# Optimization experiments

Measured on AMD Instinct MI355X. Metric: run time of the kernel, lower is better.

The kernel has to match this reference:

```python
import jax, jax.numpy as jnp
import numpy as np

EPS = 1e-14  # clamp floor from torch .clamp(1e-14)


def setup_inputs() -> dict:
    key = jax.random.key(0)
    kq, kk, kv, km = jax.random.split(key, 4)
    B, L, D = 16, 2048, 64
    q = jax.random.normal(kq, (B, L, D), dtype=jnp.float32)
    k = jax.random.normal(kk, (B, L, D), dtype=jnp.float32)
    v = jax.random.normal(kv, (B, L, D), dtype=jnp.float32)
    # boolean mask, True = masked-out position (score forced to 0 in 'dot' mode)
    attn_mask = jax.random.randint(km, (B, L, L), 0, 2).astype(jnp.bool_)
    return {"q": q, "k": k, "v": v, "attn_mask": attn_mask}


def reference(q, k, v, attn_mask):
    # kernel_type='dot': raw QK^T scores (no temperature scaling)
    attn = jnp.einsum('bqd,bkd->bqk', q, k)
    # masked positions set to 0 (not -inf) in the 'dot' path
    attn = jnp.where(attn_mask, jnp.zeros((), attn.dtype), attn)
    # sum-normalization instead of softmax: attn / attn.sum(-1).clamp(1e-14)
    denom = jnp.clip(jnp.sum(attn, axis=2, keepdims=True), EPS)
    attn = attn / denom
    # dropout is identity at inference (eval mode)
    output = jnp.einsum('bqk,bkd->bqd', attn, v)
    return output, attn
```

## Files before the change

### kernel.cpp

```cpp
#include <hip/hip_runtime.h>

#define Bb 16
#define Lq 2048
#define Dd 64
#define QT 32
#define NT 512
#define NWIN 16
#define WINB 32768

typedef _Float16 f16x2 __attribute__((ext_vector_type(2)));
typedef _Float16 f16x8 __attribute__((ext_vector_type(8)));
typedef __attribute__((ext_vector_type(4))) float f32x4;
typedef __attribute__((ext_vector_type(2))) float f32x2;
typedef __attribute__((ext_vector_type(4))) unsigned int u32x4;
typedef __attribute__((ext_vector_type(2))) unsigned int u32x2;
typedef __attribute__((ext_vector_type(4))) int i32x4;
typedef unsigned long long u64;
typedef __attribute__((ext_vector_type(2))) unsigned long long u64x2;

union H8 { f16x8 v8; f16x2 h2[4]; unsigned int u[4]; u32x4 u4; };
union H1 { f16x2 h; unsigned int u; };

__device__ __forceinline__ f16x2 pkrtz(float a, float b) {
  return __builtin_bit_cast(f16x2, __builtin_amdgcn_cvt_pkrtz(a, b));
}
__device__ __forceinline__ f32x4 MF16(f16x8 a, f16x8 b, f32x4 c) {
  return __builtin_amdgcn_mfma_f32_16x16x32_f16(a, b, c, 0, 0, 0);
}
__device__ __forceinline__ f32x4 MFu(u32x4 a, const H8& b, f32x4 c) {
  return MF16(__builtin_bit_cast(f16x8, a), b.v8, c);
}
__device__ __forceinline__ void gl_lds16(const void* g, void* l) {
  __builtin_amdgcn_global_load_lds(
      (const __attribute__((address_space(1))) void*)g,
      (__attribute__((address_space(3))) void*)l, 16, 0, 0);
}

__global__ __launch_bounds__(256)
void sdpa_prep(const float* __restrict__ kg, const float* __restrict__ vg,
               const i32x4* __restrict__ mg4,
               u32x4* __restrict__ Kw4, u32x4* __restrict__ Vq,
               u64* __restrict__ mb)
{
  const int t = threadIdx.x, blk = blockIdx.x;
  if (blk < 1024) {
    const int row = blk * 32 + (t >> 3);
    const int oct = t & 7;
    const int b = row >> 11, r = row & 2047;
    const int win = r >> 7, rw = r & 127;
    const float* kp = kg + (size_t)row * Dd + oct * 8;
    f32x4 a = *(const f32x4*)kp;
    f32x4 c = *(const f32x4*)(kp + 4);
    H1 h0, h1, h2, h3, l0, l1, l2, l3;
    h0.h = pkrtz(a.x, a.y); l0.h = pkrtz(a.x - (float)h0.h.x, a.y - (float)h0.h.y);
    h1.h = pkrtz(a.z, a.w); l1.h = pkrtz(a.z - (float)h1.h.x, a.w - (float)h1.h.y);
    h2.h = pkrtz(c.x, c.y); l2.h = pkrtz(c.x - (float)h2.h.x, c.y - (float)h2.h.y);
    h3.h = pkrtz(c.z, c.w); l3.h = pkrtz(c.z - (float)h3.h.x, c.w - (float)h3.h.y);
    u32x4 hh = {h0.u, h1.u, h2.u, h3.u};
    u32x4 ll = {l0.u, l1.u, l2.u, l3.u};
    const int sl = oct ^ (rw & 7);
    const size_t base = ((size_t)((b * 16 + win) * 128 + rw)) * 16;
    Kw4[base + sl] = hh;
    Kw4[base + 8 + sl] = ll;
  } else if (blk < 2048) {
    const int v_ = (blk - 1024) * 256 + t;
    const int ln = v_ & 15, nt = (v_ >> 4) & 3, u = (v_ >> 6) & 3;
    const int g = (v_ >> 8) & 7, w = (v_ >> 11) & 7, b = v_ >> 14;
    const int R = w * 256 + g * 32 + u * 4;
    const float* vp = vg + ((size_t)b * Lq + R) * Dd + nt * 16 + ln;
    H1 p0, p1, p2, p3;
    p0.h = pkrtz(vp[0 * Dd],  vp[1 * Dd]);
    p1.h = pkrtz(vp[2 * Dd],  vp[3 * Dd]);
    p2.h = pkrtz(vp[16 * Dd], vp[17 * Dd]);
    p3.h = pkrtz(vp[18 * Dd], vp[19 * Dd]);
    u32x4 o = {p0.u, p1.u, p2.u, p3.u};
    Vq[v_] = o;
  } else {
    const int l  = t & 63;
    const int wg = ((blk - 2048) << 2) | (t >> 6);
    i32x4 cur = __builtin_nontemporal_load(&mg4[((size_t)wg * 32) * 64 + l]);
#pragma unroll 1
    for (int it = 0; it < 32; ++it) {
      i32x4 nxt = {0, 0, 0, 0};
      if (it < 31) nxt = __builtin_nontemporal_load(&mg4[((size_t)wg * 32 + it + 1) * 64 + l]);
      u64 b0 = __ballot(cur.x != 0);
      u64 b1 = __ballot(cur.y != 0);
      u64 b2 = __ballot(cur.z != 0);
      u64 b3 = __ballot(cur.w != 0);
      if (l == 0) {
        u64* o = mb + ((size_t)wg * 32 + it) * 4;
        u64x2 w0 = {b0, b1}, w1 = {b2, b3};
        *(u64x2*)o = w0;
        *(u64x2*)(o + 2) = w1;
      }
      cur = nxt;
    }
  }
}

__global__ __launch_bounds__(NT, 4)
void sdpa_main(const float* __restrict__ qg, const char* __restrict__ Kw,
               const u32x4* __restrict__ Vqp, const u64* __restrict__ mbp,
               float* __restrict__ outO, float* __restrict__ outA)
{
  __shared__ char kbuf[2][WINB];
  __shared__ unsigned int Qh[QT][36], Ql[QT][36];
  __shared__ float red[QT][4];
  __shared__ float dinv_s[QT];

  const int tid = threadIdx.x;
  const int l   = tid & 63;
  const int ln  = l & 15;
  const int u   = l >> 4;
  const int w   = tid >> 6;
  const int qt  = w >> 2;
  const int ks  = w & 3;
  const int bid = (int)(blockIdx.x % 8) * 128 + (int)(blockIdx.x / 8);
  const int b   = bid >> 6;
  const int q0  = (bid & 63) * QT;

  {
    int r = tid >> 4, i4 = tid & 15;
    f32x4 qv = *(const f32x4*)(qg + (size_t)(b * Lq + q0 + r) * Dd + 4 * i4);
    H1 ha, hb, la, lb;
    ha.h = pkrtz(qv.x, qv.y); la.h = pkrtz(qv.x - (float)ha.h.x, qv.y - (float)ha.h.y);
    hb.h = pkrtz(qv.z, qv.w); lb.h = pkrtz(qv.z - (float)hb.h.x, qv.w - (float)hb.h.y);
    Qh[r][2 * i4] = ha.u; Qh[r][2 * i4 + 1] = hb.u;
    Ql[r][2 * i4] = la.u; Ql[r][2 * i4 + 1] = lb.u;
  }

  const char* kwb = Kw + (size_t)b * NWIN * WINB;
  auto STAGE = [&](int buf_, int win_) {
#pragma unroll
    for (int i = 0; i < 4; ++i)
      gl_lds16(kwb + (size_t)win_ * WINB + i * 8192 + w * 1024 + l * 16,
               &kbuf[buf_][i * 8192 + w * 1024]);
  };
  STAGE(0, 0);
  __syncthreads();

  H8 Bh0, Bh1, Bl0, Bl1;
  Bh0.u4 = *(const u32x4*)&Qh[16 * qt + ln][4 * u];
  Bh1.u4 = *(const u32x4*)&Qh[16 * qt + ln][16 + 4 * u];
  Bl0.u4 = *(const u32x4*)&Ql[16 * qt + ln][4 * u];
  Bl1.u4 = *(const u32x4*)&Ql[16 * qt + ln][16 + 4 * u];

  const u64* mrow = mbp + (size_t)(b * Lq + q0 + 16 * qt + ln) * 32;
  unsigned int su[NWIN][2][2];
  f32x4 pv[4] = {{0,0,0,0},{0,0,0,0},{0,0,0,0},{0,0,0,0}};
  float rs = 0.f;
  const int key   = ln & 7;
  const int rbase = ks * 32;
  u32x4 MA, MC;

#pragma unroll
  for (int win = 0; win < NWIN; ++win) {
    const int cur = win & 1;
    if (win < NWIN - 1) STAGE(cur ^ 1, win + 1);

    if ((win & 1) == 0) {
      MA = *(const u32x4*)(mrow + (win >> 1) * 4);
      MC = *(const u32x4*)(mrow + (win >> 1) * 4 + 2);
    }
    unsigned mw0 = (win & 1) ? MA.y : MA.x;
    unsigned mw1 = (win & 1) ? MA.w : MA.z;
    unsigned mw2 = (win & 1) ? MC.y : MC.x;
    unsigned mw3 = (win & 1) ? MC.w : MC.z;

    u32x4 vbuf[4];
    {
      const u32x4* vq = Vqp + (size_t)(b * 8 + (win >> 1)) * 2048;
      const int g_old = (win & 1) * 4 + ks;
#pragma unroll
      for (int nt = 0; nt < 4; ++nt)
        vbuf[nt] = vq[((g_old * 4 + u) * 4 + nt) * 16 + ln];
    }

    const char* kb_ = &kbuf[cur][0];
#pragma unroll
    for (int t = 0; t < 2; ++t) {
      const int rw = rbase + 16 * t + ln;
      const char* rp = kb_ + rw * 256;
      u32x4 h0  = *(const u32x4*)(rp + ((u ^ key) << 4));
      u32x4 h1  = *(const u32x4*)(rp + (((4 + u) ^ key) << 4));
      u32x4 l0_ = *(const u32x4*)(rp + ((8 | (u ^ key)) << 4));
      u32x4 l1_ = *(const u32x4*)(rp + ((8 | ((4 + u) ^ key)) << 4));
      f32x4 acc = {0.f, 0.f, 0.f, 0.f};
      acc = MFu(h0, Bh0, acc);
      acc = MFu(h0, Bl0, acc);
      acc = MFu(l0_, Bh0, acc);
      acc = MFu(h1, Bh1, acc);
      acc = MFu(h1, Bl1, acc);
      acc = MFu(l1_, Bh1, acc);
      const int sh = ks * 8 + 4 * t + u;
      float s0 = ((mw0 >> sh) & 1u) ? 0.f : acc.x;
      float s1 = ((mw1 >> sh) & 1u) ? 0.f : acc.y;
      float s2 = ((mw2 >> sh) & 1u) ? 0.f : acc.z;
      float s3 = ((mw3 >> sh) & 1u) ? 0.f : acc.w;
      rs += (s0 + s1) + (s2 + s3);
      H1 p0, p1;
      p0.h = pkrtz(s0, s1); p1.h = pkrtz(s2, s3);
      su[win][t][0] = p0.u; su[win][t][1] = p1.u;
    }
    {
      H8 aw;
      aw.u[0] = su[win][0][0]; aw.u[1] = su[win][0][1];
      aw.u[2] = su[win][1][0]; aw.u[3] = su[win][1][1];
      pv[0] = MF16(aw.v8, __builtin_bit_cast(f16x8, vbuf[0]), pv[0]);
      pv[1] = MF16(aw.v8, __builtin_bit_cast(f16x8, vbuf[1]), pv[1]);
      pv[2] = MF16(aw.v8, __builtin_bit_cast(f16x8, vbuf[2]), pv[2]);
      pv[3] = MF16(aw.v8, __builtin_bit_cast(f16x8, vbuf[3]), pv[3]);
    }
    __syncthreads();
  }

  rs += __shfl_xor(rs, 16);
  rs += __shfl_xor(rs, 32);
  if (l < 16) red[16 * qt + ln][ks] = rs;
  __syncthreads();
  if (tid < 32) {
    f32x4 r4 = *(const f32x4*)&red[tid][0];
    float s = (r4.x + r4.y) + (r4.z + r4.w);
    dinv_s[tid] = 1.0f / fmaxf(s, 1e-14f);
  }
  __syncthreads();

  char* Sb = &kbuf[0][0];
#pragma unroll
  for (int half = 0; half < 2; ++half) {
    if (qt == half) {
      char* srow = Sb + ln * 4096;
      const unsigned skey = (unsigned)ln << 3;
#pragma unroll
      for (int win = 0; win < NWIN; ++win)
#pragma unroll
        for (int t = 0; t < 2; ++t) {
          unsigned Bo = 256u * win + 64u * ks + 32u * t + 8u * u;
          u32x2 pk2 = {su[win][t][0], su[win][t][1]};
          *(u32x2*)(srow + (Bo ^ skey)) = pk2;
        }
    }
    __syncthreads();
#pragma unroll
    for (int r = 0; r < 2; ++r) {
      const int rl = 2 * w + r;
      const int rr = 16 * half + rl;
      const float dv = dinv_s[rr];
      const char* sr = Sb + rl * 4096;
      const unsigned rk = (unsigned)rl << 3;
      float* arow = outA + (size_t)(b * Lq + q0 + rr) * Lq;
#pragma unroll
      for (int m = 0; m < 8; ++m) {
        u32x2 pk = *(const u32x2*)(sr + ((unsigned)(512 * m + 8 * l) ^ rk));
        H1 a0, a1; a0.u = pk.x; a1.u = pk.y;
        f32x4 st = {(float)a0.h.x * dv, (float)a0.h.y * dv,
                    (float)a1.h.x * dv, (float)a1.h.y * dv};
        __builtin_nontemporal_store(st, (f32x4*)(arow + 256 * m + 4 * l));
      }
    }
    __syncthreads();
  }

  {
    float (*Or)[4][16][66] = (float (*)[4][16][66])&kbuf[0][0];
#pragma unroll
    for (int nt = 0; nt < 4; ++nt)
#pragma unroll
      for (int r2 = 0; r2 < 4; ++r2)
        Or[qt][ks][4 * u + r2][16 * nt + ln] = pv[nt][r2];
    __syncthreads();
#pragma unroll
    for (int i = 0; i < 2; ++i) {
      int item = tid + NT * i;
      int q_ = item >> 5, d = (item & 31) * 2;
      float o0 = 0.f, o1 = 0.f;
#pragma unroll
      for (int k2 = 0; k2 < 4; ++k2) {
        o0 += Or[q_ >> 4][k2][q_ & 15][d];
        o1 += Or[q_ >> 4][k2][q_ & 15][d + 1];
      }
      float dvq = dinv_s[q_];
      f32x2 st = {o0 * dvq, o1 * dvq};
      *(f32x2*)(outO + (size_t)(b * Lq + q0 + q_) * Dd + d) = st;
    }
  }
}

extern "C" void kernel_launch(void* const* d_in, const int* in_sizes, int n_in,
                              void* d_out, int out_size, void* d_ws, size_t ws_size,
                              hipStream_t stream) {
  const float* q = (const float*)d_in[0];
  const float* k = (const float*)d_in[1];
  const float* v = (const float*)d_in[2];
  const int*   m = (const int*)d_in[3];
  float* outO = (float*)d_out;
  float* outA = outO + (size_t)Bb * Lq * Dd;

  char* ws = (char*)d_ws;
  u32x4* Kw4 = (u32x4*)ws;
  u32x4* Vq  = (u32x4*)(ws + (8u << 20));
  u64*   mb  = (u64*)(ws + (12u << 20));
  sdpa_prep<<<4096, 256, 0, stream>>>(k, v, (const i32x4*)m, Kw4, Vq, mb);
  sdpa_main<<<Bb * (Lq / QT), NT, 0, stream>>>(q, (const char*)Kw4, Vq, mb, outO, outA);
}
```

Baseline: 169.7 us.

## Fuse mask bit-packing into main kernel and halve query tile to 16 rows

Mask-to-bitmask conversion moves out of the prep kernel and into the main kernel. Each block now ballots its own mask rows into shared memory, which removes the workspace round trip for the packed mask. The query tile shrinks from 32 to 16 rows, so all 8 waves split the keys of a single 16-row tile and the grid doubles. The V layout is re-permuted to match the new key split, and the PV MFMA now accumulates across pairs of windows. The trade-off is that each K window is staged and reused by fewer query rows, which doubles total K traffic from L2 into LDS.

```diff
diff --git a/kernel.cpp b/kernel.cpp
--- a/kernel.cpp
+++ b/kernel.cpp
@@ -3,7 +3,7 @@
 #define Bb 16
 #define Lq 2048
 #define Dd 64
-#define QT 32
+#define QT 16
 #define NT 512
 #define NWIN 16
 #define WINB 32768
@@ -16,7 +16,6 @@
 typedef __attribute__((ext_vector_type(2))) unsigned int u32x2;
 typedef __attribute__((ext_vector_type(4))) int i32x4;
 typedef unsigned long long u64;
-typedef __attribute__((ext_vector_type(2))) unsigned long long u64x2;
 
 union H8 { f16x8 v8; f16x2 h2[4]; unsigned int u[4]; u32x4 u4; };
 union H1 { f16x2 h; unsigned int u; };
@@ -38,9 +37,7 @@
 
 __global__ __launch_bounds__(256)
 void sdpa_prep(const float* __restrict__ kg, const float* __restrict__ vg,
-               const i32x4* __restrict__ mg4,
-               u32x4* __restrict__ Kw4, u32x4* __restrict__ Vq,
-               u64* __restrict__ mb)
+               u32x4* __restrict__ Kw4, u32x4* __restrict__ Vq)
 {
   const int t = threadIdx.x, blk = blockIdx.x;
   if (blk < 1024) {
@@ -62,71 +59,54 @@
     const size_t base = ((size_t)((b * 16 + win) * 128 + rw)) * 16;
     Kw4[base + sl] = hh;
     Kw4[base + 8 + sl] = ll;
-  } else if (blk < 2048) {
+  } else {
     const int v_ = (blk - 1024) * 256 + t;
     const int ln = v_ & 15, nt = (v_ >> 4) & 3, u = (v_ >> 6) & 3;
-    const int g = (v_ >> 8) & 7, w = (v_ >> 11) & 7, b = v_ >> 14;
-    const int R = w * 256 + g * 32 + u * 4;
-    const float* vp = vg + ((size_t)b * Lq + R) * Dd + nt * 16 + ln;
+    const int ks = (v_ >> 8) & 7, g = (v_ >> 11) & 7, b = v_ >> 14;
+    const int r0 = g * 256 + ks * 16 + 4 * u;
+    const float* vp = vg + ((size_t)b * Lq + r0) * Dd + nt * 16 + ln;
     H1 p0, p1, p2, p3;
-    p0.h = pkrtz(vp[0 * Dd],  vp[1 * Dd]);
-    p1.h = pkrtz(vp[2 * Dd],  vp[3 * Dd]);
-    p2.h = pkrtz(vp[16 * Dd], vp[17 * Dd]);
-    p3.h = pkrtz(vp[18 * Dd], vp[19 * Dd]);
+    p0.h = pkrtz(vp[0],        vp[64]);
+    p1.h = pkrtz(vp[128],      vp[192]);
+    p2.h = pkrtz(vp[128 * 64], vp[129 * 64]);
+    p3.h = pkrtz(vp[130 * 64], vp[131 * 64]);
     u32x4 o = {p0.u, p1.u, p2.u, p3.u};
     Vq[v_] = o;
-  } else {
-    const int l  = t & 63;
-    const int wg = ((blk - 2048) << 2) | (t >> 6);
-    i32x4 cur = __builtin_nontemporal_load(&mg4[((size_t)wg * 32) * 64 + l]);
-#pragma unroll 1
-    for (int it = 0; it < 32; ++it) {
-      i32x4 nxt = {0, 0, 0, 0};
-      if (it < 31) nxt = __builtin_nontemporal_load(&mg4[((size_t)wg * 32 + it + 1) * 64 + l]);
-      u64 b0 = __ballot(cur.x != 0);
-      u64 b1 = __ballot(cur.y != 0);
-      u64 b2 = __ballot(cur.z != 0);
-      u64 b3 = __ballot(cur.w != 0);
-      if (l == 0) {
-        u64* o = mb + ((size_t)wg * 32 + it) * 4;
-        u64x2 w0 = {b0, b1}, w1 = {b2, b3};
-        *(u64x2*)o = w0;
-        *(u64x2*)(o + 2) = w1;
-      }
-      cur = nxt;
-    }
   }
 }
 
 __global__ __launch_bounds__(NT, 4)
 void sdpa_main(const float* __restrict__ qg, const char* __restrict__ Kw,
-               const u32x4* __restrict__ Vqp, const u64* __restrict__ mbp,
+               const u32x4* __restrict__ Vqp, const i32x4* __restrict__ mg4,
                float* __restrict__ outO, float* __restrict__ outA)
 {
-  __shared__ char kbuf[2][WINB];
-  __shared__ unsigned int Qh[QT][36], Ql[QT][36];
-  __shared__ float red[QT][4];
+  __shared__ alignas(16) char kbuf[2][WINB];
+  __shared__ alignas(16) char qmbuf[4624];
+  __shared__ float red[QT][8];
   __shared__ float dinv_s[QT];
+
+  unsigned int (*Qh)[36] = (unsigned int (*)[36])qmbuf;
+  unsigned int (*Ql)[36] = (unsigned int (*)[36])(qmbuf + 2304);
+  u64 (*mbits)[34]       = (u64 (*)[34])qmbuf;
 
   const int tid = threadIdx.x;
   const int l   = tid & 63;
   const int ln  = l & 15;
   const int u   = l >> 4;
   const int w   = tid >> 6;
-  const int qt  = w >> 2;
-  const int ks  = w & 3;
-  const int bid = (int)(blockIdx.x % 8) * 128 + (int)(blockIdx.x / 8);
-  const int b   = bid >> 6;
-  const int q0  = (bid & 63) * QT;
-
-  {
-    int r = tid >> 4, i4 = tid & 15;
-    f32x4 qv = *(const f32x4*)(qg + (size_t)(b * Lq + q0 + r) * Dd + 4 * i4);
-    H1 ha, hb, la, lb;
-    ha.h = pkrtz(qv.x, qv.y); la.h = pkrtz(qv.x - (float)ha.h.x, qv.y - (float)ha.h.y);
-    hb.h = pkrtz(qv.z, qv.w); lb.h = pkrtz(qv.z - (float)hb.h.x, qv.w - (float)hb.h.y);
-    Qh[r][2 * i4] = ha.u; Qh[r][2 * i4 + 1] = hb.u;
-    Ql[r][2 * i4] = la.u; Ql[r][2 * i4 + 1] = lb.u;
+  const int bid = (int)(blockIdx.x % 8) * 256 + (int)(blockIdx.x / 8);
+  const int b   = bid >> 7;
+  const int q0  = (bid & 127) * QT;
+  const int ks  = w;
+
+  {
+    int r = tid >> 5, d2 = tid & 31;
+    f32x2 qv = *(const f32x2*)(qg + (size_t)(b * Lq + q0 + r) * Dd + 2 * d2);
+    H1 h, lo;
+    h.h  = pkrtz(qv.x, qv.y);
+    lo.h = pkrtz(qv.x - (float)h.h.x, qv.y - (float)h.h.y);
+    Qh[r][d2] = h.u;
+    Ql[r][d2] = lo.u;
   }
 
   const char* kwb = Kw + (size_t)b * NWIN * WINB;
@@ -140,18 +120,35 @@
   __syncthreads();
 
   H8 Bh0, Bh1, Bl0, Bl1;
-  Bh0.u4 = *(const u32x4*)&Qh[16 * qt + ln][4 * u];
-  Bh1.u4 = *(const u32x4*)&Qh[16 * qt + ln][16 + 4 * u];
-  Bl0.u4 = *(const u32x4*)&Ql[16 * qt + ln][4 * u];
-  Bl1.u4 = *(const u32x4*)&Ql[16 * qt + ln][16 + 4 * u];
-
-  const u64* mrow = mbp + (size_t)(b * Lq + q0 + 16 * qt + ln) * 32;
-  unsigned int su[NWIN][2][2];
+  Bh0.u4 = *(const u32x4*)&Qh[ln][4 * u];
+  Bh1.u4 = *(const u32x4*)&Qh[ln][16 + 4 * u];
+  Bl0.u4 = *(const u32x4*)&Ql[ln][4 * u];
+  Bl1.u4 = *(const u32x4*)&Ql[ln][16 + 4 * u];
+  __syncthreads();
+
+#pragma unroll
+  for (int i = 0; i < 2; ++i) {
+    const int row = 2 * w + i;
+    const size_t rbase = (size_t)(b * Lq + q0 + row) * 512;
+#pragma unroll
+    for (int W = 0; W < 8; ++W) {
+      i32x4 mm = __builtin_nontemporal_load(&mg4[rbase + W * 64 + l]);
+      u64 b0 = __ballot(mm.x != 0);
+      u64 b1 = __ballot(mm.y != 0);
+      u64 b2 = __ballot(mm.z != 0);
+      u64 b3 = __ballot(mm.w != 0);
+      if (l < 4) mbits[row][W * 4 + l] = (l == 0) ? b0 : (l == 1) ? b1 : (l == 2) ? b2 : b3;
+    }
+  }
+  __syncthreads();
+
+  unsigned int su[NWIN][2];
   f32x4 pv[4] = {{0,0,0,0},{0,0,0,0},{0,0,0,0},{0,0,0,0}};
   float rs = 0.f;
-  const int key   = ln & 7;
-  const int rbase = ks * 32;
-  u32x4 MA, MC;
+  const int key = ln & 7;
+  const int sh  = ks * 4 + u;
+  u32x4 MA = {0,0,0,0}, MC = {0,0,0,0};
+  u32x4 vbuf[4];
 
 #pragma unroll
   for (int win = 0; win < NWIN; ++win) {
@@ -159,28 +156,22 @@
     if (win < NWIN - 1) STAGE(cur ^ 1, win + 1);
 
     if ((win & 1) == 0) {
-      MA = *(const u32x4*)(mrow + (win >> 1) * 4);
-      MC = *(const u32x4*)(mrow + (win >> 1) * 4 + 2);
+      const int g = win >> 1;
+      const u64* mr = &mbits[ln][g * 4];
+      MA = *(const u32x4*)mr;
+      MC = *(const u32x4*)(mr + 2);
+      const u32x4* vq = Vqp + (size_t)b * 16384 + (((g * 8 + ks) * 4 + u) * 4) * 16 + ln;
+#pragma unroll
+      for (int nt = 0; nt < 4; ++nt) vbuf[nt] = vq[nt * 16];
     }
     unsigned mw0 = (win & 1) ? MA.y : MA.x;
     unsigned mw1 = (win & 1) ? MA.w : MA.z;
     unsigned mw2 = (win & 1) ? MC.y : MC.x;
     unsigned mw3 = (win & 1) ? MC.w : MC.z;
 
-    u32x4 vbuf[4];
     {
-      const u32x4* vq = Vqp + (size_t)(b * 8 + (win >> 1)) * 2048;
-      const int g_old = (win & 1) * 4 + ks;
-#pragma unroll
-      for (int nt = 0; nt < 4; ++nt)
-        vbuf[nt] = vq[((g_old * 4 + u) * 4 + nt) * 16 + ln];
-    }
-
-    const char* kb_ = &kbuf[cur][0];
-#pragma unroll
-    for (int t = 0; t < 2; ++t) {
-      const int rw = rbase + 16 * t + ln;
-      const char* rp = kb_ + rw * 256;
+      const int rw = ks * 16 + ln;
+      const char* rp = &kbuf[cur][0] + rw * 256;
       u32x4 h0  = *(const u32x4*)(rp + ((u ^ key) << 4));
       u32x4 h1  = *(const u32x4*)(rp + (((4 + u) ^ key) << 4));
       u32x4 l0_ = *(const u32x4*)(rp + ((8 | (u ^ key)) << 4));
@@ -192,7 +183,6 @@
       acc = MFu(h1, Bh1, acc);
       acc = MFu(h1, Bl1, acc);
       acc = MFu(l1_, Bh1, acc);
-      const int sh = ks * 8 + 4 * t + u;
       float s0 = ((mw0 >> sh) & 1u) ? 0.f : acc.x;
       float s1 = ((mw1 >> sh) & 1u) ? 0.f : acc.y;
       float s2 = ((mw2 >> sh) & 1u) ? 0.f : acc.z;
@@ -200,12 +190,12 @@
       rs += (s0 + s1) + (s2 + s3);
       H1 p0, p1;
       p0.h = pkrtz(s0, s1); p1.h = pkrtz(s2, s3);
-      su[win][t][0] = p0.u; su[win][t][1] = p1.u;
-    }
-    {
+      su[win][0] = p0.u; su[win][1] = p1.u;
+    }
+    if (win & 1) {
       H8 aw;
-      aw.u[0] = su[win][0][0]; aw.u[1] = su[win][0][1];
-      aw.u[2] = su[win][1][0]; aw.u[3] = su[win][1][1];
+      aw.u[0] = su[win - 1][0]; aw.u[1] = su[win - 1][1];
+      aw.u[2] = su[win][0];     aw.u[3] = su[win][1];
       pv[0] = MF16(aw.v8, __builtin_bit_cast(f16x8, vbuf[0]), pv[0]);
       pv[1] = MF16(aw.v8, __builtin_bit_cast(f16x8, vbuf[1]), pv[1]);
       pv[2] = MF16(aw.v8, __builtin_bit_cast(f16x8, vbuf[2]), pv[2]);
@@ -216,38 +206,34 @@
 
   rs += __shfl_xor(rs, 16);
   rs += __shfl_xor(rs, 32);
-  if (l < 16) red[16 * qt + ln][ks] = rs;
-  __syncthreads();
-  if (tid < 32) {
-    f32x4 r4 = *(const f32x4*)&red[tid][0];
-    float s = (r4.x + r4.y) + (r4.z + r4.w);
+  if (l < 16) red[l][ks] = rs;
+  {
+    char* srow = &kbuf[0][0] + ln * 4096;
+    const unsigned skey = (unsigned)ln << 3;
+#pragma unroll
+    for (int win = 0; win < NWIN; ++win) {
+      unsigned Bo = 256u * win + 32u * ks + 8u * u;
+      u32x2 pk2 = {su[win][0], su[win][1]};
+      *(u32x2*)(srow + (Bo ^ skey)) = pk2;
+    }
+  }
+  __syncthreads();
+  if (tid < QT) {
+    f32x4 r0 = *(const f32x4*)&red[tid][0];
+    f32x4 r1 = *(const f32x4*)&red[tid][4];
+    float s = ((r0.x + r0.y) + (r0.z + r0.w)) + ((r1.x + r1.y) + (r1.z + r1.w));
     dinv_s[tid] = 1.0f / fmaxf(s, 1e-14f);
   }
   __syncthreads();
 
-  char* Sb = &kbuf[0][0];
-#pragma unroll
-  for (int half = 0; half < 2; ++half) {
-    if (qt == half) {
-      char* srow = Sb + ln * 4096;
-      const unsigned skey = (unsigned)ln << 3;
-#pragma unroll
-      for (int win = 0; win < NWIN; ++win)
-#pragma unroll
-        for (int t = 0; t < 2; ++t) {
-          unsigned Bo = 256u * win + 64u * ks + 32u * t + 8u * u;
-          u32x2 pk2 = {su[win][t][0], su[win][t][1]};
-          *(u32x2*)(srow + (Bo ^ skey)) = pk2;
-        }
-    }
-    __syncthreads();
+  {
+    const char* Sb = &kbuf[0][0];
 #pragma unroll
     for (int r = 0; r < 2; ++r) {
-      const int rl = 2 * w + r;
-      const int rr = 16 * half + rl;
+      const int rr = 2 * w + r;
       const float dv = dinv_s[rr];
-      const char* sr = Sb + rl * 4096;
-      const unsigned rk = (unsigned)rl << 3;
+      const char* sr = Sb + rr * 4096;
+      const unsigned rk = (unsigned)rr << 3;
       float* arow = outA + (size_t)(b * Lq + q0 + rr) * Lq;
 #pragma unroll
       for (int m = 0; m < 8; ++m) {
@@ -258,26 +244,24 @@
         __builtin_nontemporal_store(st, (f32x4*)(arow + 256 * m + 4 * l));
       }
     }
+  }
+  __syncthreads();
+
+  {
+    float (*Or)[16][66] = (float (*)[16][66])&kbuf[0][0];
+#pragma unroll
+    for (int nt = 0; nt < 4; ++nt)
+#pragma unroll
+      for (int r2 = 0; r2 < 4; ++r2)
+        Or[ks][4 * u + r2][16 * nt + ln] = pv[nt][r2];
     __syncthreads();
-  }
-
-  {
-    float (*Or)[4][16][66] = (float (*)[4][16][66])&kbuf[0][0];
-#pragma unroll
-    for (int nt = 0; nt < 4; ++nt)
-#pragma unroll
-      for (int r2 = 0; r2 < 4; ++r2)
-        Or[qt][ks][4 * u + r2][16 * nt + ln] = pv[nt][r2];
-    __syncthreads();
-#pragma unroll
-    for (int i = 0; i < 2; ++i) {
-      int item = tid + NT * i;
-      int q_ = item >> 5, d = (item & 31) * 2;
+    {
+      int q_ = tid >> 5, d = (tid & 31) * 2;
       float o0 = 0.f, o1 = 0.f;
 #pragma unroll
-      for (int k2 = 0; k2 < 4; ++k2) {
-        o0 += Or[q_ >> 4][k2][q_ & 15][d];
-        o1 += Or[q_ >> 4][k2][q_ & 15][d + 1];
+      for (int k2 = 0; k2 < 8; ++k2) {
+        o0 += Or[k2][q_][d];
+        o1 += Or[k2][q_][d + 1];
       }
       float dvq = dinv_s[q_];
       f32x2 st = {o0 * dvq, o1 * dvq};
@@ -299,7 +283,7 @@
   char* ws = (char*)d_ws;
   u32x4* Kw4 = (u32x4*)ws;
   u32x4* Vq  = (u32x4*)(ws + (8u << 20));
-  u64*   mb  = (u64*)(ws + (12u << 20));
-  sdpa_prep<<<4096, 256, 0, stream>>>(k, v, (const i32x4*)m, Kw4, Vq, mb);
-  sdpa_main<<<Bb * (Lq / QT), NT, 0, stream>>>(q, (const char*)Kw4, Vq, mb, outO, outA);
-}
+  sdpa_prep<<<2048, 256, 0, stream>>>(k, v, Kw4, Vq);
+  sdpa_main<<<Bb * (Lq / QT), NT, 0, stream>>>(q, (const char*)Kw4, Vq,
+                                               (const i32x4*)m, outO, outA);
+}
```

After: 161.1 us. -5.1%, faster.
